# Kernel tuning notes

Hardware: AMD Instinct MI355X
Metric: run time of the kernel (lower is better)

## Reference

```python
import jax, jax.numpy as jnp
import numpy as np

T = 500_000  # sequence length
K = 16       # number of hidden states


def setup_inputs() -> dict:
    key = jax.random.key(0)
    k1, k2, k3, k4 = jax.random.split(key, 4)
    y = jax.random.normal(k1, (T,), dtype=jnp.float32)
    transition_logits = jax.random.normal(k2, (K, K), dtype=jnp.float32)
    mu = 2.0 * jax.random.normal(k3, (K,), dtype=jnp.float32)
    log_sigma = 0.1 * jax.random.normal(k4, (K,), dtype=jnp.float32)
    return {"y": y, "transition_logits": transition_logits, "mu": mu, "log_sigma": log_sigma}


def _stationary_distribution(P):
    # Solve pi P = pi, sum(pi) = 1 via least squares (normal equations: differentiable, jit-safe).
    k = P.shape[0]
    A = jnp.concatenate([P.T - jnp.eye(k, dtype=P.dtype), jnp.ones((1, k), dtype=P.dtype)], axis=0)
    b = jnp.concatenate([jnp.zeros((k,), dtype=P.dtype), jnp.ones((1,), dtype=P.dtype)])
    return jnp.linalg.solve(A.T @ A, A.T @ b)


def reference(y, transition_logits, mu, log_sigma):
    P = jax.nn.softmax(transition_logits, axis=-1)  # [K, K] row-stochastic transition matrix
    sigma = jnp.exp(log_sigma)
    # Gaussian emission densities g[t, k] = N(y_t; mu_k, sigma_k^2)
    z = (y[:, None] - mu[None, :]) / sigma[None, :]
    INV_SQRT_2PI = 0.3989422804014327
    g = jnp.exp(-0.5 * z * z) * (INV_SQRT_2PI / sigma)[None, :]  # [T, K]

    ut0 = _stationary_distribution(P)              # [K]
    g0 = g[0]
    ft0 = jnp.sum(ut0 * g0)                        # scalar
    utt0 = ut0 * g0 / ft0                          # [K]

    def step(utt_prev, gt):
        ut = utt_prev @ P                          # predictive dist [K]
        ft = jnp.sum(ut * gt)                      # normalizer
        utt = ut * gt / ft                         # filtered posterior [K]
        return utt, (ut, ft, utt)

    _, (Ut, ft_rest, Utt) = jax.lax.scan(step, utt0, g[1:])

    ut = jnp.concatenate([ut0[None, :], Ut], axis=0)       # [T, K]
    u_norm = jnp.concatenate([utt0[None, :], Utt], axis=0)  # [T, K]
    ft = jnp.concatenate([ft0[None], ft_rest], axis=0)      # [T]
    return (ut, u_norm, ft)
```

## Files before the change

kernel.cpp:

```cpp
#include <hip/hip_runtime.h>

#define CHUNK_L 16
#define WARMUP_W 16

typedef _Float16 h16;
typedef _Float16 h16x4 __attribute__((ext_vector_type(4)));
typedef float f32x4 __attribute__((ext_vector_type(4)));

static __device__ __forceinline__ f32x4 mfma16(h16x4 a, h16x4 b, f32x4 c) {
#if __has_builtin(__builtin_amdgcn_mfma_f32_16x16x16f16)
    return __builtin_amdgcn_mfma_f32_16x16x16f16(a, b, c, 0, 0, 0);
#else
    f32x4 d;
    asm volatile("v_mfma_f32_16x16x16_f16 %0, %1, %2, %3\n\ts_nop 7\n\ts_nop 7"
                 : "=v"(d) : "v"(a), "v"(b), "v"(c));
    return d;
#endif
}

__global__ __launch_bounds__(256, 4) void hmm_filter_kernel(
    const float* __restrict__ y,
    const float* __restrict__ logits,
    const float* __restrict__ mu,
    const float* __restrict__ log_sigma,
    float* __restrict__ out,
    int T, int nchunks)
{
    __shared__ float Plds[256];
    __shared__ float Ba[256];
    __shared__ float Bb[256];

    const int tid = (int)threadIdx.x;
    const int j   = tid & 15;
    const int gr  = tid >> 4;

    float l = logits[tid];
    float m = l;
    #pragma unroll
    for (int s = 1; s < 16; s <<= 1) m = fmaxf(m, __shfl_xor(m, s, 16));
    float e = __expf(l - m);
    float rs = e;
    #pragma unroll
    for (int s = 1; s < 16; s <<= 1) rs += __shfl_xor(rs, s, 16);
    float Pv = e / rs;
    Plds[tid] = Pv;
    Ba[tid]   = Pv;
    __syncthreads();

    float* cur = Ba;
    float* nxt = Bb;
    for (int itq = 0; itq < 10; ++itq) {
        float acc = 0.f;
        #pragma unroll
        for (int k = 0; k < 16; ++k)
            acc += cur[gr * 16 + k] * cur[k * 16 + j];
        float rsum = acc;
        #pragma unroll
        for (int s = 1; s < 16; s <<= 1) rsum += __shfl_xor(rsum, s, 16);
        nxt[tid] = acc / rsum;
        __syncthreads();
        float* tmp = cur; cur = nxt; nxt = tmp;
    }

    const int lane = tid & 63;
    const int col  = lane & 15;
    const int i0   = (lane >> 4) << 2;
    const int wv   = ((int)blockIdx.x << 2) + (tid >> 6);
    const int cbase = wv << 4;

    h16x4 Ahi, Alo;
    #pragma unroll
    for (int ee = 0; ee < 4; ++ee) {
        float a = Plds[(i0 + ee) * 16 + col];
        h16 hi = (h16)a;
        Ahi[ee] = hi;
        Alo[ee] = (h16)(a - (float)hi);
    }

    h16x4 bhi, blo;
    #pragma unroll
    for (int ee = 0; ee < 4; ++ee) {
        float pv = cur[i0 + ee];
        h16 hi = (h16)pv;
        bhi[ee] = hi;
        blo[ee] = (h16)(pv - (float)hi);
    }

    float isv[4], nmv[4], lcv[4];
    #pragma unroll
    for (int ee = 0; ee < 4; ++ee) {
        int st = i0 + ee;
        float is = __expf(-log_sigma[st]);
        isv[ee] = is;
        nmv[ee] = -mu[st] * is;
        lcv[ee] = __log2f(0.3989422804014327f * is);
    }
    const float K2 = -0.7213475204444817f;

    if (cbase >= nchunks) return;

    const int chunk = cbase + col;
    const bool live = chunk < nchunks;
    const bool isC0 = (chunk == 0);
    const int Tm4 = T - 4;
    const int TN  = T << 4;

    int tb = chunk * CHUNK_L - WARMUP_W;

    auto yld = [&](int t) -> float4 {
        int tc = t < 0 ? 0 : (t > Tm4 ? Tm4 : t);
        return *(const float4*)(y + tc);
    };

    float4 c4 = yld(tb);
    float4 n1 = yld(tb + 4);

    float r1 = 1.0f;

#define FSTEP(YT, WARM, DOST, UTP, UNP, FDST)  do {                       \
    f32x4 D = {0.f, 0.f, 0.f, 0.f};                                       \
    D = mfma16(Ahi, bhi, D);                                              \
    D = mfma16(Alo, bhi, D);                                              \
    D = mfma16(Ahi, blo, D);                                              \
    f32x4 eg;                                                             \
    _Pragma("unroll")                                                     \
    for (int ee = 0; ee < 4; ++ee) {                                      \
        float z  = fmaf((YT), isv[ee], nmv[ee]);                          \
        float gg = __builtin_amdgcn_exp2f(fmaf(z * z, K2, lcv[ee]));      \
        if (WARM) gg = isC0 ? 1.0f : gg;                                  \
        eg[ee] = gg * r1;                                                 \
    }                                                                     \
    f32x4 pg = D * eg;                                                    \
    float sv = (pg.x + pg.y) + (pg.z + pg.w);                             \
    sv += __shfl_xor(sv, 16);                                             \
    sv += __shfl_xor(sv, 32);                                             \
    float rv = __builtin_amdgcn_rcpf(sv);                                 \
    if ((DOST) && live) {                                                 \
        f32x4 ut = D * r1;                                                \
        f32x4 un = pg * rv;                                               \
        *(f32x4*)(UTP) = ut;                                              \
        *(f32x4*)(UNP) = un;                                              \
    }                                                                     \
    if (DOST) { FDST = sv; }                                              \
    _Pragma("unroll")                                                     \
    for (int ee = 0; ee < 4; ++ee) {                                      \
        h16 hh = (h16)pg[ee];                                             \
        bhi[ee] = hh;                                                     \
        blo[ee] = (h16)(pg[ee] - (float)hh);                              \
    }                                                                     \
    r1 = rv;                                                              \
} while (0)

    float fdummy;
    #pragma unroll 1
    for (int b = 0; b < WARMUP_W / 4; ++b) {
        float4 nn = yld(tb + 8);
        FSTEP(c4.x, true, false, out, out, fdummy);
        FSTEP(c4.y, true, false, out, out, fdummy);
        FSTEP(c4.z, true, false, out, out, fdummy);
        FSTEP(c4.w, true, false, out, out, fdummy);
        c4 = n1; n1 = nn; tb += 4;
    }
    (void)fdummy;

    float* pU = out + ((chunk * CHUNK_L) << 4) + i0;
    float* pN = pU + TN;
    float* pF = out + 2 * TN + chunk * CHUNK_L;
    f32x4 f4;

    #pragma unroll 1
    for (int b = 0; b < CHUNK_L / 4; ++b) {
        float4 nn = yld(tb + 8);
        FSTEP(c4.x, false, true, pU,      pN,      f4.x);
        FSTEP(c4.y, false, true, pU + 16, pN + 16, f4.y);
        FSTEP(c4.z, false, true, pU + 32, pN + 32, f4.z);
        FSTEP(c4.w, false, true, pU + 48, pN + 48, f4.w);
        if (lane < 16 && live) *(f32x4*)(pF) = f4;
        pU += 64; pN += 64; pF += 4;
        c4 = n1; n1 = nn; tb += 4;
    }
#undef FSTEP
}

extern "C" void kernel_launch(void* const* d_in, const int* in_sizes, int n_in,
                              void* d_out, int out_size, void* d_ws, size_t ws_size,
                              hipStream_t stream) {
    const float* y      = (const float*)d_in[0];
    const float* logits = (const float*)d_in[1];
    const float* mu     = (const float*)d_in[2];
    const float* ls     = (const float*)d_in[3];
    float* out = (float*)d_out;
    const int T = in_sizes[0];

    const int nchunks = (T + CHUNK_L - 1) / CHUNK_L;
    const int nwaves  = (nchunks + 15) / 16;
    const int blocks  = (nwaves + 3) / 4;
    hmm_filter_kernel<<<blocks, 256, 0, stream>>>(y, logits, mu, ls, out,
                                                  T, nchunks);
}
```

Before: 89.27 us.

## Stage filter outputs through LDS for coalesced global stores

Each wave now writes its per-step predictive and filtered vectors and normalizers into per-wave shared-memory tiles, then re-reads them with a chunk-contiguous lane mapping so each store covers a contiguous 64-float span of one chunk. Previously each lane stored 16-byte pieces scattered across 16 different chunks, giving poorly coalesced writes. The change adds LDS traffic and about 35KB of shared memory per block, which may reduce occupancy. No barrier separates the LDS writes and reads within a wave, so it relies on wave-level ordering.

```diff
diff --git a/kernel.cpp b/kernel.cpp
--- a/kernel.cpp
+++ b/kernel.cpp
@@ -29,6 +29,9 @@
     __shared__ float Plds[256];
     __shared__ float Ba[256];
     __shared__ float Bb[256];
+    __shared__ float SDu[4][16 * 68];
+    __shared__ float SDn[4][16 * 68];
+    __shared__ float SDf[4][16 * 20];
 
     const int tid = (int)threadIdx.x;
     const int j   = tid & 15;
@@ -65,7 +68,8 @@
     const int lane = tid & 63;
     const int col  = lane & 15;
     const int i0   = (lane >> 4) << 2;
-    const int wv   = ((int)blockIdx.x << 2) + (tid >> 6);
+    const int w    = tid >> 6;
+    const int wv   = ((int)blockIdx.x << 2) + w;
     const int cbase = wv << 4;
 
     h16x4 Ahi, Alo;
@@ -100,7 +104,6 @@
     if (cbase >= nchunks) return;
 
     const int chunk = cbase + col;
-    const bool live = chunk < nchunks;
     const bool isC0 = (chunk == 0);
     const int Tm4 = T - 4;
     const int TN  = T << 4;
@@ -117,7 +120,7 @@
 
     float r1 = 1.0f;
 
-#define FSTEP(YT, WARM, DOST, UTP, UNP, FDST)  do {                       \
+#define FSTEP(YT, WARM, DOST, TS, FDST)  do {                             \
     f32x4 D = {0.f, 0.f, 0.f, 0.f};                                       \
     D = mfma16(Ahi, bhi, D);                                              \
     D = mfma16(Alo, bhi, D);                                              \
@@ -135,13 +138,11 @@
     sv += __shfl_xor(sv, 16);                                             \
     sv += __shfl_xor(sv, 32);                                             \
     float rv = __builtin_amdgcn_rcpf(sv);                                 \
-    if ((DOST) && live) {                                                 \
-        f32x4 ut = D * r1;                                                \
-        f32x4 un = pg * rv;                                               \
-        *(f32x4*)(UTP) = ut;                                              \
-        *(f32x4*)(UNP) = un;                                              \
+    if (DOST) {                                                           \
+        *(f32x4*)(&SDu[w][col * 68 + (TS) * 16 + i0]) = D * r1;           \
+        *(f32x4*)(&SDn[w][col * 68 + (TS) * 16 + i0]) = pg * rv;          \
+        FDST = sv;                                                        \
     }                                                                     \
-    if (DOST) { FDST = sv; }                                              \
     _Pragma("unroll")                                                     \
     for (int ee = 0; ee < 4; ++ee) {                                      \
         h16 hh = (h16)pg[ee];                                             \
@@ -155,29 +156,49 @@
     #pragma unroll 1
     for (int b = 0; b < WARMUP_W / 4; ++b) {
         float4 nn = yld(tb + 8);
-        FSTEP(c4.x, true, false, out, out, fdummy);
-        FSTEP(c4.y, true, false, out, out, fdummy);
-        FSTEP(c4.z, true, false, out, out, fdummy);
-        FSTEP(c4.w, true, false, out, out, fdummy);
+        FSTEP(c4.x, true, false, 0, fdummy);
+        FSTEP(c4.y, true, false, 0, fdummy);
+        FSTEP(c4.z, true, false, 0, fdummy);
+        FSTEP(c4.w, true, false, 0, fdummy);
         c4 = n1; n1 = nn; tb += 4;
     }
     (void)fdummy;
 
-    float* pU = out + ((chunk * CHUNK_L) << 4) + i0;
-    float* pN = pU + TN;
-    float* pF = out + 2 * TN + chunk * CHUNK_L;
     f32x4 f4;
 
     #pragma unroll 1
     for (int b = 0; b < CHUNK_L / 4; ++b) {
         float4 nn = yld(tb + 8);
-        FSTEP(c4.x, false, true, pU,      pN,      f4.x);
-        FSTEP(c4.y, false, true, pU + 16, pN + 16, f4.y);
-        FSTEP(c4.z, false, true, pU + 32, pN + 32, f4.z);
-        FSTEP(c4.w, false, true, pU + 48, pN + 48, f4.w);
-        if (lane < 16 && live) *(f32x4*)(pF) = f4;
-        pU += 64; pN += 64; pF += 4;
+        FSTEP(c4.x, false, true, 0, f4.x);
+        FSTEP(c4.y, false, true, 1, f4.y);
+        FSTEP(c4.z, false, true, 2, f4.z);
+        FSTEP(c4.w, false, true, 3, f4.w);
+        if (lane < 16)
+            *(f32x4*)(&SDf[w][col * 20 + b * 4]) = f4;
+
+        #pragma unroll
+        for (int i = 0; i < 4; ++i) {
+            const int cl  = i * 4 + (lane >> 4);
+            const int off = lane & 15;
+            f32x4 vu = *(f32x4*)(&SDu[w][cl * 68 + off * 4]);
+            f32x4 vn = *(f32x4*)(&SDn[w][cl * 68 + off * 4]);
+            const int cc = cbase + cl;
+            if (cc < nchunks) {
+                float* dst = out + (size_t)cc * 256 + b * 64 + off * 4;
+                *(f32x4*)dst        = vu;
+                *(f32x4*)(dst + TN) = vn;
+            }
+        }
         c4 = n1; n1 = nn; tb += 4;
+    }
+
+    {
+        const int cc = cbase + (lane >> 2);
+        if (cc < nchunks) {
+            f32x4 fv = *(f32x4*)(&SDf[w][(lane >> 2) * 20 + (lane & 3) * 4]);
+            float* dst = out + 2 * (size_t)TN + (size_t)cbase * 16 + lane * 4;
+            *(f32x4*)dst = fv;
+        }
     }
 #undef FSTEP
 }
```

Measured after the change: 89.98 us. Within noise of the previous version (+0.8%).
